# Performance work log

Hardware: AMD Instinct MI355X
Metric: run time of the kernel (lower is better)

The kernel has to match this reference:

```python
import jax, jax.numpy as jnp
import numpy as np

B, S, D, H = 4, 2048, 768, 12
HD = D // H
SCALE = HD ** -0.5


def setup_inputs() -> dict:
    key = jax.random.key(0)
    ks = jax.random.split(key, 10)
    inp = {
        "x": jax.random.normal(ks[0], (B, S, D), jnp.float32),
        "attn_mask": jax.random.normal(ks[1], (B, S), jnp.float32),
        "Wq": jax.random.normal(ks[2], (D, D), jnp.float32) * (D ** -0.5),
        "bq": jax.random.normal(ks[3], (D,), jnp.float32) * 0.02,
        "Wk": jax.random.normal(ks[4], (D, D), jnp.float32) * (D ** -0.5),
        "bk": jax.random.normal(ks[5], (D,), jnp.float32) * 0.02,
        "Wv": jax.random.normal(ks[6], (D, D), jnp.float32) * (D ** -0.5),
        "bv": jax.random.normal(ks[7], (D,), jnp.float32) * 0.02,
        "Wo": jax.random.normal(ks[8], (D, D), jnp.float32) * (D ** -0.5),
        "bo": jax.random.normal(ks[9], (D,), jnp.float32) * 0.02,
    }
    return inp


def _split_heads(e):
    # [B, S, D] -> [B, H, S, HD]
    return e.reshape(B, S, H, HD).transpose(0, 2, 1, 3)


def reference(x, attn_mask, Wq, bq, Wk, bk, Wv, bv, Wo, bo):
    q = _split_heads((x @ Wq + bq) * SCALE)          # [B,H,S,HD]
    k = _split_heads(x @ Wk + bk)                     # [B,H,S,HD]
    v = _split_heads(x @ Wv + bv)                     # [B,H,S,HD]
    scores = jnp.einsum('bhsd,bhtd->bhst', q, k)      # [B,H,S,S]
    scores = scores + attn_mask[:, None, None, :]     # additive mask over keys
    probs = jax.nn.softmax(scores, axis=-1)
    out = jnp.einsum('bhst,bhtd->bhsd', probs, v)     # [B,H,S,HD]
    out = out.transpose(0, 2, 1, 3).reshape(B, S, D)  # merge heads
    return out @ Wo + bo
```

## Files before the change

kernel.cpp:

```cpp
#include <hip/hip_runtime.h>
#include <cmath>

#define B_ 4
#define S_ 2048
#define D_ 768
#define H_ 12
#define HD_ 64
#define SCALE_ 0.125f
#define LOG2E_ 1.4426950408889634f
#define M_ 8192

typedef unsigned short ushortT;
typedef __attribute__((ext_vector_type(8))) __bf16 bf16x8;
typedef __attribute__((ext_vector_type(4))) float f32x4;

typedef __attribute__((address_space(1))) const void glb_cv;
typedef __attribute__((address_space(3))) void lds_v;

__device__ inline ushortT f2bf(float f) {
    return __builtin_bit_cast(ushortT, (__bf16)f);
}

__device__ inline void gload_lds16(const void* g, void* l) {
    __builtin_amdgcn_global_load_lds((glb_cv*)g, (lds_v*)l, 16, 0, 0);
}

__global__ __launch_bounds__(256)
void convert_f32_bf16(const float* __restrict__ in, ushortT* __restrict__ out)
{
    const size_t i = ((size_t)blockIdx.x * 256 + threadIdx.x) * 8;
    float4 a = *(const float4*)(in + i);
    float4 b = *(const float4*)(in + i + 4);
    union { ushortT u[8]; float4 f; } o;
    o.u[0] = f2bf(a.x); o.u[1] = f2bf(a.y); o.u[2] = f2bf(a.z); o.u[3] = f2bf(a.w);
    o.u[4] = f2bf(b.x); o.u[5] = f2bf(b.y); o.u[6] = f2bf(b.z); o.u[7] = f2bf(b.w);
    *(float4*)(out + i) = o.f;
}

__global__ __launch_bounds__(256)
void transpose_w(const float* __restrict__ W0, const float* __restrict__ W1,
                 const float* __restrict__ W2, const float* __restrict__ W3,
                 ushortT* __restrict__ wt4)
{
    const float* W = (blockIdx.z == 0) ? W0 : (blockIdx.z == 1) ? W1
                   : (blockIdx.z == 2) ? W2 : W3;
    ushortT* o = wt4 + (size_t)blockIdx.z * 768 * 768;
    __shared__ float T[64][65];
    const int tid = threadIdx.x;
    const int k0 = blockIdx.x * 64, n0 = blockIdx.y * 64;

    for (int t = tid; t < 1024; t += 256) {
        const int r = t >> 4, c4 = (t & 15) << 2;
        float4 v = *(const float4*)&W[(size_t)(k0 + r) * 768 + n0 + c4];
        T[r][c4 + 0] = v.x; T[r][c4 + 1] = v.y;
        T[r][c4 + 2] = v.z; T[r][c4 + 3] = v.w;
    }
    __syncthreads();
    for (int t = tid; t < 1024; t += 256) {
        const int r = t >> 4, c4 = (t & 15) << 2;
        union { ushortT u[4]; unsigned long long v; } ov;
        ov.u[0] = f2bf(T[c4 + 0][r]); ov.u[1] = f2bf(T[c4 + 1][r]);
        ov.u[2] = f2bf(T[c4 + 2][r]); ov.u[3] = f2bf(T[c4 + 3][r]);
        *(unsigned long long*)&o[(size_t)(n0 + r) * 768 + k0 + c4] = ov.v;
    }
}

__device__ inline void gemm_core_128x64(
    const ushortT* __restrict__ A, const ushortT* __restrict__ Bt,
    ushortT* As, ushortT* Bs, int m0, int n0, f32x4 acc[4][2])
{
    const int tid  = threadIdx.x;
    const int lane = tid & 63;
    const int wave = tid >> 6;
    const int lr = lane & 15, lg = lane >> 4;
    const int wr = wave >> 1, wc = wave & 1;

    #pragma unroll
    for (int mi = 0; mi < 4; ++mi)
        #pragma unroll
        for (int ni = 0; ni < 2; ++ni)
            acc[mi][ni] = (f32x4){0.f, 0.f, 0.f, 0.f};

    #pragma unroll 1
    for (int k0 = 0; k0 < 768; k0 += 64) {
        __syncthreads();
        #pragma unroll
        for (int it = 0; it < 4; ++it) {
            const int ci = it * 256 + tid;
            const int row = ci >> 3, c = ci & 7;
            const int sc = c ^ (row & 7);
            gload_lds16(A + (size_t)(m0 + row) * 768 + k0 + sc * 8,
                        As + (size_t)(it * 256 + wave * 64) * 8);
        }
        #pragma unroll
        for (int it = 0; it < 2; ++it) {
            const int ci = it * 256 + tid;
            const int row = ci >> 3, c = ci & 7;
            const int sc = c ^ (row & 7);
            gload_lds16(Bt + (size_t)(n0 + row) * 768 + k0 + sc * 8,
                        Bs + (size_t)(it * 256 + wave * 64) * 8);
        }
        __syncthreads();

        #pragma unroll
        for (int ks = 0; ks < 2; ++ks) {
            bf16x8 af[4], bfr[2];
            #pragma unroll
            for (int mi = 0; mi < 4; ++mi) {
                const int row = wr * 64 + mi * 16 + lr;
                const int ch = (ks * 4 + lg) ^ (row & 7);
                af[mi] = __builtin_bit_cast(bf16x8, *(const float4*)(As + row * 64 + ch * 8));
            }
            #pragma unroll
            for (int ni = 0; ni < 2; ++ni) {
                const int row = wc * 32 + ni * 16 + lr;
                const int ch = (ks * 4 + lg) ^ (row & 7);
                bfr[ni] = __builtin_bit_cast(bf16x8, *(const float4*)(Bs + row * 64 + ch * 8));
            }
            #pragma unroll
            for (int mi = 0; mi < 4; ++mi)
                #pragma unroll
                for (int ni = 0; ni < 2; ++ni)
                    acc[mi][ni] = __builtin_amdgcn_mfma_f32_16x16x32_bf16(
                        af[mi], bfr[ni], acc[mi][ni], 0, 0, 0);
        }
    }
}

__global__ __launch_bounds__(256)
void qkv_gemm(const ushortT* __restrict__ xb, const ushortT* __restrict__ wt4,
              const float* __restrict__ bq, const float* __restrict__ bk,
              const float* __restrict__ bv,
              ushortT* __restrict__ qb, ushortT* __restrict__ kb,
              ushortT* __restrict__ vb)
{
    __shared__ __align__(16) ushortT As[128 * 64];
    __shared__ __align__(16) ushortT Bs[64 * 64];
    const int z = blockIdx.z;
    const ushortT* Wt = wt4 + (size_t)z * 768 * 768;
    const float* bias = (z == 0) ? bq : (z == 1) ? bk : bv;
    ushortT* out = (z == 0) ? qb : (z == 1) ? kb : vb;
    const float scale = (z == 0) ? (SCALE_ * LOG2E_) : 1.0f;

    const int m0 = blockIdx.x * 128, n0 = blockIdx.y * 64;
    f32x4 acc[4][2];
    gemm_core_128x64(xb, Wt, As, Bs, m0, n0, acc);

    const int tid = threadIdx.x;
    const int lane = tid & 63, wave = tid >> 6;
    const int lr = lane & 15, lg = lane >> 4;
    const int wr = wave >> 1, wc = wave & 1;
    const int h = n0 >> 6;

    #pragma unroll
    for (int ni = 0; ni < 2; ++ni) {
        const int nn = wc * 32 + ni * 16 + lr;
        const float bb = bias[n0 + nn];
        #pragma unroll
        for (int mi = 0; mi < 4; ++mi) {
            #pragma unroll
            for (int j = 0; j < 4; ++j) {
                const int m = m0 + wr * 64 + mi * 16 + lg * 4 + j;
                const int b = m >> 11, s = m & 2047;
                out[(((size_t)b * H_ + h) * S_ + s) * HD_ + nn] =
                    f2bf((acc[mi][ni][j] + bb) * scale);
            }
        }
    }
}

__global__ __launch_bounds__(256)
void o_gemm(const ushortT* __restrict__ ab, const ushortT* __restrict__ wto,
            const float* __restrict__ bo, float* __restrict__ out)
{
    __shared__ __align__(16) ushortT As[128 * 64];
    __shared__ __align__(16) ushortT Bs[64 * 64];
    const int m0 = blockIdx.x * 128, n0 = blockIdx.y * 64;
    f32x4 acc[4][2];
    gemm_core_128x64(ab, wto, As, Bs, m0, n0, acc);

    const int tid = threadIdx.x;
    const int lane = tid & 63, wave = tid >> 6;
    const int lr = lane & 15, lg = lane >> 4;
    const int wr = wave >> 1, wc = wave & 1;

    #pragma unroll
    for (int ni = 0; ni < 2; ++ni) {
        const int n = n0 + wc * 32 + ni * 16 + lr;
        const float bb = bo[n];
        #pragma unroll
        for (int mi = 0; mi < 4; ++mi) {
            #pragma unroll
            for (int j = 0; j < 4; ++j) {
                const int m = m0 + wr * 64 + mi * 16 + lg * 4 + j;
                out[(size_t)m * 768 + n] = acc[mi][ni][j] + bb;
            }
        }
    }
}

__global__ __launch_bounds__(256)
void transpose_v(const ushortT* __restrict__ V, ushortT* __restrict__ Vt)
{
    __shared__ __align__(16) ushortT T[64 * 68];
    const int tid = threadIdx.x;
    const size_t bh = (size_t)blockIdx.z * H_ + blockIdx.y;
    const int s0 = blockIdx.x * 64;

    for (int t2 = tid; t2 < 512; t2 += 256) {
        const int row = t2 >> 3, c = t2 & 7;
        *(float4*)&T[row * 68 + c * 8] =
            *(const float4*)&V[(bh * S_ + s0 + row) * HD_ + c * 8];
    }
    __syncthreads();
    for (int t2 = tid; t2 < 512; t2 += 256) {
        const int hd = t2 >> 3, c = t2 & 7;
        union { ushortT u[8]; float4 f; } tmp;
        #pragma unroll
        for (int i = 0; i < 8; ++i) tmp.u[i] = T[(c * 8 + i) * 68 + hd];
        *(float4*)&Vt[(bh * HD_ + hd) * S_ + s0 + c * 8] = tmp.f;
    }
}

__global__ __launch_bounds__(256)
void attn_mfma(const ushortT* __restrict__ Q, const ushortT* __restrict__ K,
               const ushortT* __restrict__ Vt, const float* __restrict__ mask,
               ushortT* __restrict__ out)
{
    __shared__ __align__(16) ushortT Ks[2][64 * 64];
    __shared__ __align__(16) ushortT Vs[2][64 * 64];
    __shared__ __align__(16) ushortT Ps[4][16 * 88];
    __shared__ float Ms[S_];

    const int tid  = threadIdx.x;
    const int lane = tid & 63;
    const int wave = tid >> 6;
    const int lr   = lane & 15;
    const int lg   = lane >> 4;

    const int gid  = blockIdx.x;
    const int xcd  = gid & 7;
    const int w    = gid >> 3;
    const int bh_i = xcd * 6 + (w >> 4);
    const int q0   = (w & 15) * 128;
    const int b    = bh_i / H_;
    const int h    = bh_i % H_;
    const size_t bh = (size_t)bh_i;

    for (int f = tid; f < 512; f += 256) {
        float4 mv = *(const float4*)&mask[(size_t)b * S_ + f * 4];
        mv.x *= LOG2E_; mv.y *= LOG2E_; mv.z *= LOG2E_; mv.w *= LOG2E_;
        *(float4*)&Ms[f * 4] = mv;
    }

    bf16x8 qf[2][2];
    #pragma unroll
    for (int g = 0; g < 2; ++g) {
        const ushortT* Qg = Q + (bh * S_ + q0 + wave * 32 + g * 16 + lr) * HD_;
        qf[g][0] = __builtin_bit_cast(bf16x8, *(const float4*)(Qg + lg * 8));
        qf[g][1] = __builtin_bit_cast(bf16x8, *(const float4*)(Qg + 32 + lg * 8));
    }

    const ushortT* Kg = K  + bh * S_ * HD_;
    const ushortT* Vg = Vt + bh * HD_ * S_;

    bf16x8 ones;
    #pragma unroll
    for (int i = 0; i < 8; ++i) ones[i] = (__bf16)1.0f;

    f32x4 acc[2][4];
    f32x4 accl[2];
    #pragma unroll
    for (int g = 0; g < 2; ++g) {
        #pragma unroll
        for (int cb = 0; cb < 4; ++cb) acc[g][cb] = (f32x4){0.f, 0.f, 0.f, 0.f};
        accl[g] = (f32x4){0.f, 0.f, 0.f, 0.f};
    }

    auto stage = [&](int bsel, int k0) {
        #pragma unroll
        for (int it = 0; it < 2; ++it) {
            const int ci = it * 256 + tid;
            const int row = ci >> 3, c = ci & 7, sc = c ^ (row & 7);
            gload_lds16(Kg + (size_t)(k0 + row) * HD_ + sc * 8,
                        &Ks[bsel][(it * 256 + wave * 64) * 8]);
        }
        #pragma unroll
        for (int it = 0; it < 2; ++it) {
            const int ci = it * 256 + tid;
            const int row = ci >> 3, c = ci & 7, sc = c ^ (row & 7);
            gload_lds16(Vg + (size_t)row * S_ + k0 + sc * 8,
                        &Vs[bsel][(it * 256 + wave * 64) * 8]);
        }
    };

    stage(0, 0);
    __syncthreads();

    for (int kt = 0; kt < S_ / 64; ++kt) {
        const int k0 = kt * 64;
        const int buf = kt & 1;
        if (kt + 1 < S_ / 64) stage(buf ^ 1, k0 + 64);

        bf16x8 kf[4][2];
        #pragma unroll
        for (int cb = 0; cb < 4; ++cb) {
            #pragma unroll
            for (int ks = 0; ks < 2; ++ks) {
                const int rk = cb * 16 + lr;
                const int pp = (ks * 4 + lg) ^ (rk & 7);
                kf[cb][ks] = __builtin_bit_cast(bf16x8,
                    *(const float4*)(&Ks[buf][rk * 64 + pp * 8]));
            }
        }
        f32x4 mv[4];
        #pragma unroll
        for (int cb = 0; cb < 4; ++cb)
            mv[cb] = __builtin_bit_cast(f32x4,
                *(const float4*)&Ms[k0 + cb * 16 + lg * 4]);

        bf16x8 vf[4][2];
        #pragma unroll
        for (int cb = 0; cb < 4; ++cb) {
            #pragma unroll
            for (int ks2 = 0; ks2 < 2; ++ks2) {
                const int rv = cb * 16 + lr;
                const int pp = (ks2 * 4 + lg) ^ (rv & 7);
                vf[cb][ks2] = __builtin_bit_cast(bf16x8,
                    *(const float4*)(&Vs[buf][rv * 64 + pp * 8]));
            }
        }

        #pragma unroll
        for (int g = 0; g < 2; ++g) {
            f32x4 s[4];
            #pragma unroll
            for (int cb = 0; cb < 4; ++cb) s[cb] = mv[cb];
            __builtin_amdgcn_s_setprio(1);
            #pragma unroll
            for (int cb = 0; cb < 4; ++cb)
                #pragma unroll
                for (int ks = 0; ks < 2; ++ks)
                    s[cb] = __builtin_amdgcn_mfma_f32_16x16x32_bf16(
                        kf[cb][ks], qf[g][ks], s[cb], 0, 0, 0);
            __builtin_amdgcn_s_setprio(0);

            ushort4 pw[4];
            #pragma unroll
            for (int cb = 0; cb < 4; ++cb) {
                pw[cb].x = f2bf(exp2f(s[cb][0]));
                pw[cb].y = f2bf(exp2f(s[cb][1]));
                pw[cb].z = f2bf(exp2f(s[cb][2]));
                pw[cb].w = f2bf(exp2f(s[cb][3]));
            }
            #pragma unroll
            for (int cb = 0; cb < 4; ++cb)
                *(ushort4*)&Ps[wave][lr * 88 + cb * 16 + lg * 4] = pw[cb];

            bf16x8 pf[2];
            #pragma unroll
            for (int ks2 = 0; ks2 < 2; ++ks2)
                pf[ks2] = __builtin_bit_cast(bf16x8,
                    *(const float4*)(&Ps[wave][lr * 88 + ks2 * 32 + lg * 8]));
            __builtin_amdgcn_s_setprio(1);
            #pragma unroll
            for (int ks2 = 0; ks2 < 2; ++ks2) {
                #pragma unroll
                for (int cb = 0; cb < 4; ++cb)
                    acc[g][cb] = __builtin_amdgcn_mfma_f32_16x16x32_bf16(
                        pf[ks2], vf[cb][ks2], acc[g][cb], 0, 0, 0);
                accl[g] = __builtin_amdgcn_mfma_f32_16x16x32_bf16(
                    pf[ks2], ones, accl[g], 0, 0, 0);
            }
            __builtin_amdgcn_s_setprio(0);
        }

        __syncthreads();
    }

    #pragma unroll
    for (int g = 0; g < 2; ++g) {
        f32x4 inv;
        #pragma unroll
        for (int j = 0; j < 4; ++j) inv[j] = 1.f / accl[g][j];
        #pragma unroll
        for (int cb = 0; cb < 4; ++cb) {
            #pragma unroll
            for (int j = 0; j < 4; ++j) {
                const size_t row = (size_t)b * S_ + q0 + wave * 32 + g * 16 + lg * 4 + j;
                out[row * D_ + h * HD_ + cb * 16 + lr] = f2bf(acc[g][cb][j] * inv[j]);
            }
        }
    }
}

extern "C" void kernel_launch(void* const* d_in, const int* in_sizes, int n_in,
                              void* d_out, int out_size, void* d_ws, size_t ws_size,
                              hipStream_t stream)
{
    const float* x    = (const float*)d_in[0];
    const float* mask = (const float*)d_in[1];
    const float* Wq   = (const float*)d_in[2];
    const float* bq   = (const float*)d_in[3];
    const float* Wk   = (const float*)d_in[4];
    const float* bk   = (const float*)d_in[5];
    const float* Wv   = (const float*)d_in[6];
    const float* bv   = (const float*)d_in[7];
    const float* Wo   = (const float*)d_in[8];
    const float* bo   = (const float*)d_in[9];
    float* out = (float*)d_out;

    const size_t NE = (size_t)B_ * S_ * D_;
    ushortT* xb  = (ushortT*)d_ws;
    ushortT* qb  = xb + NE;
    ushortT* kb  = qb + NE;
    ushortT* vb  = kb + NE;
    ushortT* vtb = vb + NE;
    ushortT* ab  = vtb + NE;
    ushortT* wt4 = ab + NE;

    convert_f32_bf16<<<NE / 2048, 256, 0, stream>>>(x, xb);
    transpose_w<<<dim3(12, 12, 4), 256, 0, stream>>>(Wq, Wk, Wv, Wo, wt4);

    qkv_gemm<<<dim3(M_ / 128, 12, 3), 256, 0, stream>>>(
        xb, wt4, bq, bk, bv, qb, kb, vb);

    transpose_v<<<dim3(S_ / 64, H_, B_), 256, 0, stream>>>(vb, vtb);

    attn_mfma<<<768, 256, 0, stream>>>(qb, kb, vtb, mask, ab);

    o_gemm<<<dim3(M_ / 128, 12), 256, 0, stream>>>(
        ab, wt4 + 3 * 768 * 768, bo, out);
}
```

Before: 187.4 us.

## Fuse V transpose into QKV epilogue and keep P in registers for attention

The QKV GEMM epilogue now writes V directly in transposed [B,H,HD,S] layout, which removes the separate transpose_v kernel and its extra memory round trip. The attention kernel is restructured to 128 threads with 64 query rows per wave. Instead of passing the softmax probabilities through LDS, it feeds them straight into 16x16x16 MFMAs in the transposed orientation, which removes the LDS writes, reads and padding buffer for P. The trade-offs are more registers per wave, a different block size and occupancy, and half-width MFMAs for the PV product.

```diff
diff --git a/kernel.cpp b/kernel.cpp
--- a/kernel.cpp
+++ b/kernel.cpp
@@ -12,7 +12,9 @@
 
 typedef unsigned short ushortT;
 typedef __attribute__((ext_vector_type(8))) __bf16 bf16x8;
+typedef __attribute__((ext_vector_type(4))) __bf16 bf16x4;
 typedef __attribute__((ext_vector_type(4))) float f32x4;
+typedef __attribute__((ext_vector_type(4))) short s16x4;
 
 typedef __attribute__((address_space(1))) const void glb_cv;
 typedef __attribute__((address_space(3))) void lds_v;
@@ -23,6 +25,18 @@
 
 __device__ inline void gload_lds16(const void* g, void* l) {
     __builtin_amdgcn_global_load_lds((glb_cv*)g, (lds_v*)l, 16, 0, 0);
+}
+
+__device__ inline f32x4 mfma16(bf16x4 a, bf16x4 b, f32x4 c) {
+#if __has_builtin(__builtin_amdgcn_mfma_f32_16x16x16_bf16)
+    return __builtin_amdgcn_mfma_f32_16x16x16_bf16(a, b, c, 0, 0, 0);
+#elif __has_builtin(__builtin_amdgcn_mfma_f32_16x16x16bf16_1k)
+    return __builtin_amdgcn_mfma_f32_16x16x16bf16_1k(
+        __builtin_bit_cast(s16x4, a), __builtin_bit_cast(s16x4, b), c, 0, 0, 0);
+#else
+    asm("v_mfma_f32_16x16x16_bf16 %0, %1, %2, %0" : "+v"(c) : "v"(a), "v"(b));
+    return c;
+#endif
 }
 
 __global__ __launch_bounds__(256)
@@ -132,14 +146,13 @@
               const float* __restrict__ bq, const float* __restrict__ bk,
               const float* __restrict__ bv,
               ushortT* __restrict__ qb, ushortT* __restrict__ kb,
-              ushortT* __restrict__ vb)
+              ushortT* __restrict__ vtb)
 {
     __shared__ __align__(16) ushortT As[128 * 64];
     __shared__ __align__(16) ushortT Bs[64 * 64];
     const int z = blockIdx.z;
     const ushortT* Wt = wt4 + (size_t)z * 768 * 768;
     const float* bias = (z == 0) ? bq : (z == 1) ? bk : bv;
-    ushortT* out = (z == 0) ? qb : (z == 1) ? kb : vb;
     const float scale = (z == 0) ? (SCALE_ * LOG2E_) : 1.0f;
 
     const int m0 = blockIdx.x * 128, n0 = blockIdx.y * 64;
@@ -152,18 +165,38 @@
     const int wr = wave >> 1, wc = wave & 1;
     const int h = n0 >> 6;
 
-    #pragma unroll
-    for (int ni = 0; ni < 2; ++ni) {
-        const int nn = wc * 32 + ni * 16 + lr;
-        const float bb = bias[n0 + nn];
-        #pragma unroll
-        for (int mi = 0; mi < 4; ++mi) {
-            #pragma unroll
-            for (int j = 0; j < 4; ++j) {
-                const int m = m0 + wr * 64 + mi * 16 + lg * 4 + j;
-                const int b = m >> 11, s = m & 2047;
-                out[(((size_t)b * H_ + h) * S_ + s) * HD_ + nn] =
-                    f2bf((acc[mi][ni][j] + bb) * scale);
+    if (z == 2) {
+        #pragma unroll
+        for (int ni = 0; ni < 2; ++ni) {
+            const int nn = wc * 32 + ni * 16 + lr;
+            const float bb = bias[n0 + nn];
+            #pragma unroll
+            for (int mi = 0; mi < 4; ++mi) {
+                const int mb = m0 + wr * 64 + mi * 16 + lg * 4;
+                const int b = mb >> 11, s = mb & 2047;
+                ushort4 ov;
+                ov.x = f2bf(acc[mi][ni][0] + bb);
+                ov.y = f2bf(acc[mi][ni][1] + bb);
+                ov.z = f2bf(acc[mi][ni][2] + bb);
+                ov.w = f2bf(acc[mi][ni][3] + bb);
+                *(ushort4*)&vtb[(((size_t)b * H_ + h) * HD_ + nn) * S_ + s] = ov;
+            }
+        }
+    } else {
+        ushortT* out = (z == 0) ? qb : kb;
+        #pragma unroll
+        for (int ni = 0; ni < 2; ++ni) {
+            const int nn = wc * 32 + ni * 16 + lr;
+            const float bb = bias[n0 + nn];
+            #pragma unroll
+            for (int mi = 0; mi < 4; ++mi) {
+                #pragma unroll
+                for (int j = 0; j < 4; ++j) {
+                    const int m = m0 + wr * 64 + mi * 16 + lg * 4 + j;
+                    const int b = m >> 11, s = m & 2047;
+                    out[(((size_t)b * H_ + h) * S_ + s) * HD_ + nn] =
+                        f2bf((acc[mi][ni][j] + bb) * scale);
+                }
             }
         }
     }
@@ -199,37 +232,13 @@
     }
 }
 
-__global__ __launch_bounds__(256)
-void transpose_v(const ushortT* __restrict__ V, ushortT* __restrict__ Vt)
-{
-    __shared__ __align__(16) ushortT T[64 * 68];
-    const int tid = threadIdx.x;
-    const size_t bh = (size_t)blockIdx.z * H_ + blockIdx.y;
-    const int s0 = blockIdx.x * 64;
-
-    for (int t2 = tid; t2 < 512; t2 += 256) {
-        const int row = t2 >> 3, c = t2 & 7;
-        *(float4*)&T[row * 68 + c * 8] =
-            *(const float4*)&V[(bh * S_ + s0 + row) * HD_ + c * 8];
-    }
-    __syncthreads();
-    for (int t2 = tid; t2 < 512; t2 += 256) {
-        const int hd = t2 >> 3, c = t2 & 7;
-        union { ushortT u[8]; float4 f; } tmp;
-        #pragma unroll
-        for (int i = 0; i < 8; ++i) tmp.u[i] = T[(c * 8 + i) * 68 + hd];
-        *(float4*)&Vt[(bh * HD_ + hd) * S_ + s0 + c * 8] = tmp.f;
-    }
-}
-
-__global__ __launch_bounds__(256)
+__global__ __launch_bounds__(128, 2)
 void attn_mfma(const ushortT* __restrict__ Q, const ushortT* __restrict__ K,
                const ushortT* __restrict__ Vt, const float* __restrict__ mask,
                ushortT* __restrict__ out)
 {
     __shared__ __align__(16) ushortT Ks[2][64 * 64];
     __shared__ __align__(16) ushortT Vs[2][64 * 64];
-    __shared__ __align__(16) ushortT Ps[4][16 * 88];
     __shared__ float Ms[S_];
 
     const int tid  = threadIdx.x;
@@ -247,16 +256,16 @@
     const int h    = bh_i % H_;
     const size_t bh = (size_t)bh_i;
 
-    for (int f = tid; f < 512; f += 256) {
+    for (int f = tid; f < 512; f += 128) {
         float4 mv = *(const float4*)&mask[(size_t)b * S_ + f * 4];
         mv.x *= LOG2E_; mv.y *= LOG2E_; mv.z *= LOG2E_; mv.w *= LOG2E_;
         *(float4*)&Ms[f * 4] = mv;
     }
 
-    bf16x8 qf[2][2];
-    #pragma unroll
-    for (int g = 0; g < 2; ++g) {
-        const ushortT* Qg = Q + (bh * S_ + q0 + wave * 32 + g * 16 + lr) * HD_;
+    bf16x8 qf[4][2];
+    #pragma unroll
+    for (int g = 0; g < 4; ++g) {
+        const ushortT* Qg = Q + (bh * S_ + q0 + wave * 64 + g * 16 + lr) * HD_;
         qf[g][0] = __builtin_bit_cast(bf16x8, *(const float4*)(Qg + lg * 8));
         qf[g][1] = __builtin_bit_cast(bf16x8, *(const float4*)(Qg + 32 + lg * 8));
     }
@@ -264,14 +273,14 @@
     const ushortT* Kg = K  + bh * S_ * HD_;
     const ushortT* Vg = Vt + bh * HD_ * S_;
 
-    bf16x8 ones;
-    #pragma unroll
-    for (int i = 0; i < 8; ++i) ones[i] = (__bf16)1.0f;
-
-    f32x4 acc[2][4];
-    f32x4 accl[2];
-    #pragma unroll
-    for (int g = 0; g < 2; ++g) {
+    bf16x4 onesA;
+    #pragma unroll
+    for (int i = 0; i < 4; ++i) onesA[i] = (__bf16)1.0f;
+
+    f32x4 acc[4][4];
+    f32x4 accl[4];
+    #pragma unroll
+    for (int g = 0; g < 4; ++g) {
         #pragma unroll
         for (int cb = 0; cb < 4; ++cb) acc[g][cb] = (f32x4){0.f, 0.f, 0.f, 0.f};
         accl[g] = (f32x4){0.f, 0.f, 0.f, 0.f};
@@ -279,18 +288,18 @@
 
     auto stage = [&](int bsel, int k0) {
         #pragma unroll
-        for (int it = 0; it < 2; ++it) {
-            const int ci = it * 256 + tid;
+        for (int it = 0; it < 4; ++it) {
+            const int ci = it * 128 + tid;
             const int row = ci >> 3, c = ci & 7, sc = c ^ (row & 7);
             gload_lds16(Kg + (size_t)(k0 + row) * HD_ + sc * 8,
-                        &Ks[bsel][(it * 256 + wave * 64) * 8]);
-        }
-        #pragma unroll
-        for (int it = 0; it < 2; ++it) {
-            const int ci = it * 256 + tid;
+                        &Ks[bsel][(it * 128 + wave * 64) * 8]);
+        }
+        #pragma unroll
+        for (int it = 0; it < 4; ++it) {
+            const int ci = it * 128 + tid;
             const int row = ci >> 3, c = ci & 7, sc = c ^ (row & 7);
             gload_lds16(Vg + (size_t)row * S_ + k0 + sc * 8,
-                        &Vs[bsel][(it * 256 + wave * 64) * 8]);
+                        &Vs[bsel][(it * 128 + wave * 64) * 8]);
         }
     };
 
@@ -319,77 +328,69 @@
             mv[cb] = __builtin_bit_cast(f32x4,
                 *(const float4*)&Ms[k0 + cb * 16 + lg * 4]);
 
-        bf16x8 vf[4][2];
-        #pragma unroll
-        for (int cb = 0; cb < 4; ++cb) {
-            #pragma unroll
-            for (int ks2 = 0; ks2 < 2; ++ks2) {
-                const int rv = cb * 16 + lr;
-                const int pp = (ks2 * 4 + lg) ^ (rv & 7);
-                vf[cb][ks2] = __builtin_bit_cast(bf16x8,
-                    *(const float4*)(&Vs[buf][rv * 64 + pp * 8]));
-            }
-        }
-
-        #pragma unroll
-        for (int g = 0; g < 2; ++g) {
+        bf16x4 vf[4][4];
+        #pragma unroll
+        for (int cbh = 0; cbh < 4; ++cbh) {
+            const int rv = cbh * 16 + lr;
+            #pragma unroll
+            for (int sl = 0; sl < 4; ++sl) {
+                const int cg = sl * 2 + (lg >> 1);
+                const int cl = cg ^ (rv & 7);
+                vf[cbh][sl] = __builtin_bit_cast(bf16x4,
+                    *(const ulonglong1*)(&Vs[buf][rv * 64 + cl * 8 + (lg & 1) * 4]));
+            }
+        }
+
+        #pragma unroll
+        for (int g = 0; g < 4; ++g) {
             f32x4 s[4];
-            #pragma unroll
-            for (int cb = 0; cb < 4; ++cb) s[cb] = mv[cb];
             __builtin_amdgcn_s_setprio(1);
             #pragma unroll
-            for (int cb = 0; cb < 4; ++cb)
+            for (int cb = 0; cb < 4; ++cb) {
+                s[cb] = __builtin_amdgcn_mfma_f32_16x16x32_bf16(
+                    kf[cb][0], qf[g][0], mv[cb], 0, 0, 0);
+                s[cb] = __builtin_amdgcn_mfma_f32_16x16x32_bf16(
+                    kf[cb][1], qf[g][1], s[cb], 0, 0, 0);
+            }
+            __builtin_amdgcn_s_setprio(0);
+
+            bf16x4 pb[4];
+            #pragma unroll
+            for (int cb = 0; cb < 4; ++cb) {
+                pb[cb][0] = (__bf16)exp2f(s[cb][0]);
+                pb[cb][1] = (__bf16)exp2f(s[cb][1]);
+                pb[cb][2] = (__bf16)exp2f(s[cb][2]);
+                pb[cb][3] = (__bf16)exp2f(s[cb][3]);
+            }
+
+            __builtin_amdgcn_s_setprio(1);
+            #pragma unroll
+            for (int sl = 0; sl < 4; ++sl) {
                 #pragma unroll
-                for (int ks = 0; ks < 2; ++ks)
-                    s[cb] = __builtin_amdgcn_mfma_f32_16x16x32_bf16(
-                        kf[cb][ks], qf[g][ks], s[cb], 0, 0, 0);
+                for (int cbh = 0; cbh < 4; ++cbh)
+                    acc[g][cbh] = mfma16(vf[cbh][sl], pb[sl], acc[g][cbh]);
+                accl[g] = mfma16(onesA, pb[sl], accl[g]);
+            }
             __builtin_amdgcn_s_setprio(0);
-
-            ushort4 pw[4];
-            #pragma unroll
-            for (int cb = 0; cb < 4; ++cb) {
-                pw[cb].x = f2bf(exp2f(s[cb][0]));
-                pw[cb].y = f2bf(exp2f(s[cb][1]));
-                pw[cb].z = f2bf(exp2f(s[cb][2]));
-                pw[cb].w = f2bf(exp2f(s[cb][3]));
-            }
-            #pragma unroll
-            for (int cb = 0; cb < 4; ++cb)
-                *(ushort4*)&Ps[wave][lr * 88 + cb * 16 + lg * 4] = pw[cb];
-
-            bf16x8 pf[2];
-            #pragma unroll
-            for (int ks2 = 0; ks2 < 2; ++ks2)
-                pf[ks2] = __builtin_bit_cast(bf16x8,
-                    *(const float4*)(&Ps[wave][lr * 88 + ks2 * 32 + lg * 8]));
-            __builtin_amdgcn_s_setprio(1);
-            #pragma unroll
-            for (int ks2 = 0; ks2 < 2; ++ks2) {
-                #pragma unroll
-                for (int cb = 0; cb < 4; ++cb)
-                    acc[g][cb] = __builtin_amdgcn_mfma_f32_16x16x32_bf16(
-                        pf[ks2], vf[cb][ks2], acc[g][cb], 0, 0, 0);
-                accl[g] = __builtin_amdgcn_mfma_f32_16x16x32_bf16(
-                    pf[ks2], ones, accl[g], 0, 0, 0);
-            }
-            __builtin_amdgcn_s_setprio(0);
         }
 
         __syncthreads();
     }
 
-    #pragma unroll
-    for (int g = 0; g < 2; ++g) {
-        f32x4 inv;
-        #pragma unroll
-        for (int j = 0; j < 4; ++j) inv[j] = 1.f / accl[g][j];
-        #pragma unroll
-        for (int cb = 0; cb < 4; ++cb) {
-            #pragma unroll
-            for (int j = 0; j < 4; ++j) {
-                const size_t row = (size_t)b * S_ + q0 + wave * 32 + g * 16 + lg * 4 + j;
-                out[row * D_ + h * HD_ + cb * 16 + lr] = f2bf(acc[g][cb][j] * inv[j]);
-            }
+    asm volatile("s_nop 7\n\ts_nop 7" ::: );
+
+    #pragma unroll
+    for (int g = 0; g < 4; ++g) {
+        const float inv = 1.f / accl[g][0];
+        const size_t row = (size_t)b * S_ + q0 + wave * 64 + g * 16 + lr;
+        #pragma unroll
+        for (int cbh = 0; cbh < 4; ++cbh) {
+            ushort4 ov;
+            ov.x = f2bf(acc[g][cbh][0] * inv);
+            ov.y = f2bf(acc[g][cbh][1] * inv);
+            ov.z = f2bf(acc[g][cbh][2] * inv);
+            ov.w = f2bf(acc[g][cbh][3] * inv);
+            *(ushort4*)&out[row * D_ + h * HD_ + cbh * 16 + lg * 4] = ov;
         }
     }
 }
@@ -414,8 +415,7 @@
     ushortT* xb  = (ushortT*)d_ws;
     ushortT* qb  = xb + NE;
     ushortT* kb  = qb + NE;
-    ushortT* vb  = kb + NE;
-    ushortT* vtb = vb + NE;
+    ushortT* vtb = kb + NE;
     ushortT* ab  = vtb + NE;
     ushortT* wt4 = ab + NE;
 
@@ -423,11 +423,9 @@
     transpose_w<<<dim3(12, 12, 4), 256, 0, stream>>>(Wq, Wk, Wv, Wo, wt4);
 
     qkv_gemm<<<dim3(M_ / 128, 12, 3), 256, 0, stream>>>(
-        xb, wt4, bq, bk, bv, qb, kb, vb);
-
-    transpose_v<<<dim3(S_ / 64, H_, B_), 256, 0, stream>>>(vb, vtb);
-
-    attn_mfma<<<768, 256, 0, stream>>>(qb, kb, vtb, mask, ab);
+        xb, wt4, bq, bk, bv, qb, kb, vtb);
+
+    attn_mfma<<<768, 128, 0, stream>>>(qb, kb, vtb, mask, ab);
 
     o_gemm<<<dim3(M_ / 128, 12), 256, 0, stream>>>(
         ab, wt4 + 3 * 768 * 768, bo, out);
```

Result: no change. 187.2 us (-0.1%).
